# Kernel optimization log

Measured on AMD Instinct MI355X. Metric: run time of the kernel, lower is better.

Reference implementation:

```python
import jax, jax.numpy as jnp
import numpy as np

HSIZE = 128
E = 640000


def _init_linear(key, fan_in, fan_out):
    # torch nn.Linear default init: U(-1/sqrt(fan_in), 1/sqrt(fan_in))
    kw, kb = jax.random.split(key)
    bound = 1.0 / np.sqrt(fan_in)
    W = jax.random.uniform(kw, (fan_in, fan_out), jnp.float32, -bound, bound)
    b = jax.random.uniform(kb, (fan_out,), jnp.float32, -bound, bound)
    return W, b


def setup_inputs() -> dict:
    key = jax.random.key(0)
    ks = jax.random.split(key, 6)
    hself = jax.random.normal(ks[0], (E, HSIZE), jnp.float32)
    hother = jax.random.normal(ks[1], (E, HSIZE), jnp.float32)
    Wm1, bm1 = _init_linear(ks[2], 2 * HSIZE, HSIZE)
    Wm2, bm2 = _init_linear(ks[3], HSIZE, HSIZE)
    Wu1, bu1 = _init_linear(ks[4], 2 * HSIZE, HSIZE)
    Wu2, bu2 = _init_linear(ks[5], HSIZE, HSIZE)
    return {"hself": hself, "hother": hother,
            "Wm1": Wm1, "bm1": bm1, "Wm2": Wm2, "bm2": bm2,
            "Wu1": Wu1, "bu1": bu1, "Wu2": Wu2, "bu2": bu2}


def _mlp2(a, b, W1, b1, W2, b2):
    # concat([a, b], -1) @ W1 done without materializing the concat
    h = a @ W1[:HSIZE] + b @ W1[HSIZE:] + b1
    h = jax.nn.relu(h)
    return h @ W2 + b2


def reference(hself, hother, Wm1, bm1, Wm2, bm2, Wu1, bu1, Wu2, bu2):
    # msg: Linear(2h,h) -> ReLU -> Linear(h,h) on cat([hself, hother])
    msg = _mlp2(hself, hother, Wm1, bm1, Wm2, bm2)
    # upd: Linear(2h,h) -> ReLU -> Linear(h,h) on cat([hself, msg])
    out = _mlp2(hself, msg, Wu1, bu1, Wu2, bu2)
    return out
```

## Files before the change

kernel.cpp:

```cpp
#include <hip/hip_runtime.h>

typedef __bf16 bf16_t;
typedef __bf16 bf16x8 __attribute__((ext_vector_type(8)));
typedef float f32x4 __attribute__((ext_vector_type(4)));

#define MFMA(a, b, c) __builtin_amdgcn_mfma_f32_16x16x32_bf16((a), (b), (c), 0, 0, 0)

#define E_ROWS 640000
#define BM 128

static __device__ __forceinline__ bf16x8 cvt8(float4 a, float4 b) {
  bf16x8 r;
  r[0] = (bf16_t)a.x; r[1] = (bf16_t)a.y; r[2] = (bf16_t)a.z; r[3] = (bf16_t)a.w;
  r[4] = (bf16_t)b.x; r[5] = (bf16_t)b.y; r[6] = (bf16_t)b.z; r[7] = (bf16_t)b.w;
  return r;
}

__global__ __launch_bounds__(256) void prep_weights(
    const float* __restrict__ Wm1, const float* __restrict__ Wm2,
    const float* __restrict__ Wu1, const float* __restrict__ Wu2,
    bf16_t* __restrict__ wt) {
  int c = blockIdx.x * 256 + threadIdx.x;
  if (c >= 12288) return;
  int lane = c & 63, f = c >> 6;
  const float* W; int base;
  if (f < 64)       { W = Wm1; base = 0;   }
  else if (f < 96)  { W = Wm2; base = 64;  }
  else if (f < 160) { W = Wu1; base = 96;  }
  else              { W = Wu2; base = 160; }
  int fl = f - base;
  int ks = fl >> 3, nb = fl & 7;
  int k0 = 32 * ks + 8 * (lane >> 4);
  int n  = 16 * nb + (lane & 15);
  bf16x8 v;
  #pragma unroll
  for (int j = 0; j < 8; ++j) v[j] = (bf16_t)W[(size_t)(k0 + j) * 128 + n];
  ((bf16x8*)wt)[c] = v;
}

static __device__ __forceinline__ void loadB(bf16x8* dst, const bf16x8* gb,
                                             int fragbase, int lane) {
  #pragma unroll
  for (int n = 0; n < 8; ++n) dst[n] = gb[(size_t)(fragbase + n) * 64 + lane];
}

__global__ __launch_bounds__(256, 2) void fused_mp(
    const float* __restrict__ hself, const float* __restrict__ hother,
    const bf16_t* __restrict__ wt,
    const float* __restrict__ bm1, const float* __restrict__ bm2,
    const float* __restrict__ bu1, const float* __restrict__ bu2,
    float* __restrict__ out) {
  __shared__ bf16_t conv[128 * 128];

  const int tid = threadIdx.x;
  const int lane = tid & 63;
  const int wave = tid >> 6;
  const int col16 = lane & 15;
  const int kgrp = lane >> 4;
  const int rowloc0 = wave * 32;
  const int swz = (col16 & 7) << 4;

  const bf16x8* gb = (const bf16x8*)wt;

  float bm1v[8], bm2v[8], bu1v[8], bu2v[8];
  #pragma unroll
  for (int n = 0; n < 8; ++n) {
    bm1v[n] = bm1[n * 16 + col16];
    bm2v[n] = bm2[n * 16 + col16];
    bu1v[n] = bu1[n * 16 + col16];
    bu2v[n] = bu2[n * 16 + col16];
  }

  bf16x8 hsf[2][4], hof[2][4];
  {
    float4 t0[2][4], t1[2][4], u0[2][4], u1[2][4];
    #pragma unroll
    for (int rb = 0; rb < 2; ++rb) {
      #pragma unroll
      for (int ks = 0; ks < 4; ++ks) {
        size_t row = (size_t)blockIdx.x * BM + rowloc0 + rb * 16 + col16;
        const float* p = hself + row * 128 + ks * 32 + kgrp * 8;
        t0[rb][ks] = *(const float4*)p;
        t1[rb][ks] = *(const float4*)(p + 4);
        const float* q = hother + row * 128 + ks * 32 + kgrp * 8;
        u0[rb][ks] = *(const float4*)q;
        u1[rb][ks] = *(const float4*)(q + 4);
      }
    }
    #pragma unroll
    for (int rb = 0; rb < 2; ++rb) {
      #pragma unroll
      for (int ks = 0; ks < 4; ++ks) {
        hsf[rb][ks] = cvt8(t0[rb][ks], t1[rb][ks]);
        hof[rb][ks] = cvt8(u0[rb][ks], u1[rb][ks]);
      }
    }
  }

  f32x4 acc[2][8];
  bf16x8 bA[8], bB[8];

  #pragma unroll
  for (int rb = 0; rb < 2; ++rb)
    #pragma unroll
    for (int n = 0; n < 8; ++n)
      acc[rb][n] = (f32x4){0.f, 0.f, 0.f, 0.f};

  loadB(bA, gb, 0, lane);
  #pragma unroll
  for (int ks = 0; ks < 8; ++ks) {
    bf16x8* bc = (ks & 1) ? bB : bA;
    bf16x8* bn = (ks & 1) ? bA : bB;
    if (ks < 7) loadB(bn, gb, (ks + 1) * 8, lane);
    bf16x8 a0 = (ks < 4) ? hsf[0][ks & 3] : hof[0][ks & 3];
    bf16x8 a1 = (ks < 4) ? hsf[1][ks & 3] : hof[1][ks & 3];
    #pragma unroll
    for (int n = 0; n < 8; ++n) {
      acc[0][n] = MFMA(a0, bc[n], acc[0][n]);
      acc[1][n] = MFMA(a1, bc[n], acc[1][n]);
    }
  }

  #pragma unroll
  for (int rb = 0; rb < 2; ++rb)
    #pragma unroll
    for (int n = 0; n < 8; ++n)
      #pragma unroll
      for (int e = 0; e < 4; ++e) {
        float v = fmaxf(acc[rb][n][e] + bm1v[n], 0.f);
        int r = rowloc0 + rb * 16 + kgrp * 4 + e;
        int byteoff = ((r << 8) + (n * 16 + col16) * 2) ^ ((r & 7) << 4);
        *(bf16_t*)((char*)conv + byteoff) = (bf16_t)v;
      }
  asm volatile("s_waitcnt lgkmcnt(0)" ::: "memory");

  bf16x8 h1f[2][4];
  #pragma unroll
  for (int rb = 0; rb < 2; ++rb)
    #pragma unroll
    for (int ks = 0; ks < 4; ++ks) {
      int r = rowloc0 + rb * 16 + col16;
      h1f[rb][ks] = *(const bf16x8*)((const char*)conv +
                    (((r << 8) + ks * 64 + kgrp * 16) ^ swz));
    }

  #pragma unroll
  for (int rb = 0; rb < 2; ++rb)
    #pragma unroll
    for (int n = 0; n < 8; ++n)
      acc[rb][n] = (f32x4){0.f, 0.f, 0.f, 0.f};

  loadB(bA, gb, 64, lane);
  #pragma unroll
  for (int ks = 0; ks < 4; ++ks) {
    bf16x8* bc = (ks & 1) ? bB : bA;
    bf16x8* bn = (ks & 1) ? bA : bB;
    if (ks < 3) loadB(bn, gb, 64 + (ks + 1) * 8, lane);
    #pragma unroll
    for (int n = 0; n < 8; ++n) {
      acc[0][n] = MFMA(h1f[0][ks], bc[n], acc[0][n]);
      acc[1][n] = MFMA(h1f[1][ks], bc[n], acc[1][n]);
    }
  }

  #pragma unroll
  for (int rb = 0; rb < 2; ++rb)
    #pragma unroll
    for (int n = 0; n < 8; ++n)
      #pragma unroll
      for (int e = 0; e < 4; ++e) {
        float v = acc[rb][n][e] + bm2v[n];
        int r = rowloc0 + rb * 16 + kgrp * 4 + e;
        int byteoff = ((r << 8) + (n * 16 + col16) * 2) ^ ((r & 7) << 4);
        *(bf16_t*)((char*)conv + byteoff) = (bf16_t)v;
      }
  asm volatile("s_waitcnt lgkmcnt(0)" ::: "memory");

  bf16x8 msgf[2][4];
  #pragma unroll
  for (int rb = 0; rb < 2; ++rb)
    #pragma unroll
    for (int ks = 0; ks < 4; ++ks) {
      int r = rowloc0 + rb * 16 + col16;
      msgf[rb][ks] = *(const bf16x8*)((const char*)conv +
                     (((r << 8) + ks * 64 + kgrp * 16) ^ swz));
    }

  #pragma unroll
  for (int rb = 0; rb < 2; ++rb)
    #pragma unroll
    for (int n = 0; n < 8; ++n)
      acc[rb][n] = (f32x4){0.f, 0.f, 0.f, 0.f};

  loadB(bA, gb, 96, lane);
  #pragma unroll
  for (int ks = 0; ks < 8; ++ks) {
    bf16x8* bc = (ks & 1) ? bB : bA;
    bf16x8* bn = (ks & 1) ? bA : bB;
    if (ks < 7) loadB(bn, gb, 96 + (ks + 1) * 8, lane);
    bf16x8 a0 = (ks < 4) ? hsf[0][ks & 3] : msgf[0][ks & 3];
    bf16x8 a1 = (ks < 4) ? hsf[1][ks & 3] : msgf[1][ks & 3];
    #pragma unroll
    for (int n = 0; n < 8; ++n) {
      acc[0][n] = MFMA(a0, bc[n], acc[0][n]);
      acc[1][n] = MFMA(a1, bc[n], acc[1][n]);
    }
  }

  #pragma unroll
  for (int rb = 0; rb < 2; ++rb)
    #pragma unroll
    for (int n = 0; n < 8; ++n)
      #pragma unroll
      for (int e = 0; e < 4; ++e) {
        float v = fmaxf(acc[rb][n][e] + bu1v[n], 0.f);
        int r = rowloc0 + rb * 16 + kgrp * 4 + e;
        int byteoff = ((r << 8) + (n * 16 + col16) * 2) ^ ((r & 7) << 4);
        *(bf16_t*)((char*)conv + byteoff) = (bf16_t)v;
      }
  asm volatile("s_waitcnt lgkmcnt(0)" ::: "memory");

  bf16x8 h2f[2][4];
  #pragma unroll
  for (int rb = 0; rb < 2; ++rb)
    #pragma unroll
    for (int ks = 0; ks < 4; ++ks) {
      int r = rowloc0 + rb * 16 + col16;
      h2f[rb][ks] = *(const bf16x8*)((const char*)conv +
                    (((r << 8) + ks * 64 + kgrp * 16) ^ swz));
    }

  #pragma unroll
  for (int rb = 0; rb < 2; ++rb)
    #pragma unroll
    for (int n = 0; n < 8; ++n)
      acc[rb][n] = (f32x4){0.f, 0.f, 0.f, 0.f};

  loadB(bA, gb, 160, lane);
  #pragma unroll
  for (int ks = 0; ks < 4; ++ks) {
    bf16x8* bc = (ks & 1) ? bB : bA;
    bf16x8* bn = (ks & 1) ? bA : bB;
    if (ks < 3) loadB(bn, gb, 160 + (ks + 1) * 8, lane);
    #pragma unroll
    for (int n = 0; n < 8; ++n) {
      acc[0][n] = MFMA(h2f[0][ks], bc[n], acc[0][n]);
      acc[1][n] = MFMA(h2f[1][ks], bc[n], acc[1][n]);
    }
  }

  #pragma unroll
  for (int rb = 0; rb < 2; ++rb)
    #pragma unroll
    for (int n = 0; n < 8; ++n)
      #pragma unroll
      for (int e = 0; e < 4; ++e) {
        size_t r = (size_t)blockIdx.x * BM + rowloc0 + rb * 16 + kgrp * 4 + e;
        out[r * 128 + n * 16 + col16] = acc[rb][n][e] + bu2v[n];
      }
}

extern "C" void kernel_launch(void* const* d_in, const int* in_sizes, int n_in,
                              void* d_out, int out_size, void* d_ws, size_t ws_size,
                              hipStream_t stream) {
  const float* hself  = (const float*)d_in[0];
  const float* hother = (const float*)d_in[1];
  const float* Wm1 = (const float*)d_in[2];
  const float* bm1 = (const float*)d_in[3];
  const float* Wm2 = (const float*)d_in[4];
  const float* bm2 = (const float*)d_in[5];
  const float* Wu1 = (const float*)d_in[6];
  const float* bu1 = (const float*)d_in[7];
  const float* Wu2 = (const float*)d_in[8];
  const float* bu2 = (const float*)d_in[9];
  float* out = (float*)d_out;
  bf16_t* wt = (bf16_t*)d_ws;

  prep_weights<<<48, 256, 0, stream>>>(Wm1, Wm2, Wu1, Wu2, wt);
  fused_mp<<<E_ROWS / BM, 256, 0, stream>>>(hself, hother, wt,
                                            bm1, bm2, bu1, bu2, out);
}
```

Measured before the change: 350.1 us.

## Swap MFMA operands to compute transposed tiles, vectorize stores and repack

Swaps the MFMA operands so each wave computes the transposed output tile, with weights as the A operand and activations as the B operand. Each lane then holds four consecutive output columns of one row. The final fp32 output is written with float4 stores instead of scalar stores. Inter-layer activations are repacked through per-wave LDS with packed 8-byte writes instead of per-element bf16 stores. Bias is folded into the accumulator initialization. The new layout must match the MFMA fragment convention exactly for the results to stay correct.

```diff
diff --git a/kernel.cpp b/kernel.cpp
--- a/kernel.cpp
+++ b/kernel.cpp
@@ -14,6 +14,12 @@
   r[0] = (bf16_t)a.x; r[1] = (bf16_t)a.y; r[2] = (bf16_t)a.z; r[3] = (bf16_t)a.w;
   r[4] = (bf16_t)b.x; r[5] = (bf16_t)b.y; r[6] = (bf16_t)b.z; r[7] = (bf16_t)b.w;
   return r;
+}
+
+static __device__ __forceinline__ unsigned int pk2(float a, float b) {
+  unsigned short ua = __builtin_bit_cast(unsigned short, (bf16_t)a);
+  unsigned short ub = __builtin_bit_cast(unsigned short, (bf16_t)b);
+  return ((unsigned int)ub << 16) | ua;
 }
 
 __global__ __launch_bounds__(256) void prep_weights(
@@ -38,10 +44,10 @@
   ((bf16x8*)wt)[c] = v;
 }
 
-static __device__ __forceinline__ void loadB(bf16x8* dst, const bf16x8* gb,
+static __device__ __forceinline__ void loadW(bf16x8* dst, const bf16x8* gb,
                                              int fragbase, int lane) {
   #pragma unroll
-  for (int n = 0; n < 8; ++n) dst[n] = gb[(size_t)(fragbase + n) * 64 + lane];
+  for (int n = 0; n < 8; ++n) dst[n] = gb[(fragbase + n) * 64 + lane];
 }
 
 __global__ __launch_bounds__(256, 2) void fused_mp(
@@ -50,214 +56,196 @@
     const float* __restrict__ bm1, const float* __restrict__ bm2,
     const float* __restrict__ bu1, const float* __restrict__ bu2,
     float* __restrict__ out) {
-  __shared__ bf16_t conv[128 * 128];
+  __shared__ bf16_t repack[4 * 4096];
 
   const int tid = threadIdx.x;
   const int lane = tid & 63;
   const int wave = tid >> 6;
-  const int col16 = lane & 15;
-  const int kgrp = lane >> 4;
-  const int rowloc0 = wave * 32;
-  const int swz = (col16 & 7) << 4;
-
+  const int c = lane & 15;
+  const int g = lane >> 4;
+
+  char* myrep = (char*)(repack + wave * 4096);
   const bf16x8* gb = (const bf16x8*)wt;
-
-  float bm1v[8], bm2v[8], bu1v[8], bu2v[8];
-  #pragma unroll
-  for (int n = 0; n < 8; ++n) {
-    bm1v[n] = bm1[n * 16 + col16];
-    bm2v[n] = bm2[n * 16 + col16];
-    bu1v[n] = bu1[n * 16 + col16];
-    bu2v[n] = bu2[n * 16 + col16];
-  }
+  const size_t rowbase = (size_t)blockIdx.x * BM + wave * 32;
 
   bf16x8 hsf[2][4], hof[2][4];
   {
     float4 t0[2][4], t1[2][4], u0[2][4], u1[2][4];
     #pragma unroll
-    for (int rb = 0; rb < 2; ++rb) {
+    for (int mt = 0; mt < 2; ++mt) {
       #pragma unroll
       for (int ks = 0; ks < 4; ++ks) {
-        size_t row = (size_t)blockIdx.x * BM + rowloc0 + rb * 16 + col16;
-        const float* p = hself + row * 128 + ks * 32 + kgrp * 8;
-        t0[rb][ks] = *(const float4*)p;
-        t1[rb][ks] = *(const float4*)(p + 4);
-        const float* q = hother + row * 128 + ks * 32 + kgrp * 8;
-        u0[rb][ks] = *(const float4*)q;
-        u1[rb][ks] = *(const float4*)(q + 4);
+        size_t row = rowbase + mt * 16 + c;
+        const float* p = hself + row * 128 + ks * 32 + g * 8;
+        t0[mt][ks] = *(const float4*)p;
+        t1[mt][ks] = *(const float4*)(p + 4);
+        const float* q = hother + row * 128 + ks * 32 + g * 8;
+        u0[mt][ks] = *(const float4*)q;
+        u1[mt][ks] = *(const float4*)(q + 4);
       }
     }
     #pragma unroll
-    for (int rb = 0; rb < 2; ++rb) {
+    for (int mt = 0; mt < 2; ++mt) {
       #pragma unroll
       for (int ks = 0; ks < 4; ++ks) {
-        hsf[rb][ks] = cvt8(t0[rb][ks], t1[rb][ks]);
-        hof[rb][ks] = cvt8(u0[rb][ks], u1[rb][ks]);
+        hsf[mt][ks] = cvt8(t0[mt][ks], t1[mt][ks]);
+        hof[mt][ks] = cvt8(u0[mt][ks], u1[mt][ks]);
       }
     }
   }
 
   f32x4 acc[2][8];
-  bf16x8 bA[8], bB[8];
-
-  #pragma unroll
-  for (int rb = 0; rb < 2; ++rb)
-    #pragma unroll
-    for (int n = 0; n < 8; ++n)
-      acc[rb][n] = (f32x4){0.f, 0.f, 0.f, 0.f};
-
-  loadB(bA, gb, 0, lane);
+  bf16x8 wA[8], wB[8];
+
+  #pragma unroll
+  for (int nb = 0; nb < 8; ++nb) {
+    float4 b4 = *(const float4*)(bm1 + nb * 16 + g * 4);
+    acc[0][nb] = (f32x4){b4.x, b4.y, b4.z, b4.w};
+    acc[1][nb] = acc[0][nb];
+  }
+  loadW(wA, gb, 0, lane);
   #pragma unroll
   for (int ks = 0; ks < 8; ++ks) {
-    bf16x8* bc = (ks & 1) ? bB : bA;
-    bf16x8* bn = (ks & 1) ? bA : bB;
-    if (ks < 7) loadB(bn, gb, (ks + 1) * 8, lane);
-    bf16x8 a0 = (ks < 4) ? hsf[0][ks & 3] : hof[0][ks & 3];
-    bf16x8 a1 = (ks < 4) ? hsf[1][ks & 3] : hof[1][ks & 3];
-    #pragma unroll
-    for (int n = 0; n < 8; ++n) {
-      acc[0][n] = MFMA(a0, bc[n], acc[0][n]);
-      acc[1][n] = MFMA(a1, bc[n], acc[1][n]);
-    }
-  }
-
-  #pragma unroll
-  for (int rb = 0; rb < 2; ++rb)
-    #pragma unroll
-    for (int n = 0; n < 8; ++n)
-      #pragma unroll
-      for (int e = 0; e < 4; ++e) {
-        float v = fmaxf(acc[rb][n][e] + bm1v[n], 0.f);
-        int r = rowloc0 + rb * 16 + kgrp * 4 + e;
-        int byteoff = ((r << 8) + (n * 16 + col16) * 2) ^ ((r & 7) << 4);
-        *(bf16_t*)((char*)conv + byteoff) = (bf16_t)v;
-      }
+    bf16x8* wc = (ks & 1) ? wB : wA;
+    bf16x8* wn = (ks & 1) ? wA : wB;
+    if (ks < 7) loadW(wn, gb, (ks + 1) * 8, lane);
+    bf16x8 x0 = (ks < 4) ? hsf[0][ks & 3] : hof[0][ks & 3];
+    bf16x8 x1 = (ks < 4) ? hsf[1][ks & 3] : hof[1][ks & 3];
+    #pragma unroll
+    for (int nb = 0; nb < 8; ++nb) {
+      acc[0][nb] = MFMA(wc[nb], x0, acc[0][nb]);
+      acc[1][nb] = MFMA(wc[nb], x1, acc[1][nb]);
+    }
+  }
+
+  #pragma unroll
+  for (int mt = 0; mt < 2; ++mt)
+    #pragma unroll
+    for (int nb = 0; nb < 8; ++nb) {
+      f32x4 v = acc[mt][nb];
+      uint2 w;
+      w.x = pk2(fmaxf(v[0], 0.f), fmaxf(v[1], 0.f));
+      w.y = pk2(fmaxf(v[2], 0.f), fmaxf(v[3], 0.f));
+      int dstlane = c + 16 * (2 * (nb & 1) + (g >> 1));
+      int off = ((mt * 4 + (nb >> 1)) * 64 + dstlane) * 16 + (g & 1) * 8;
+      *(uint2*)(myrep + off) = w;
+    }
   asm volatile("s_waitcnt lgkmcnt(0)" ::: "memory");
-
-  bf16x8 h1f[2][4];
-  #pragma unroll
-  for (int rb = 0; rb < 2; ++rb)
-    #pragma unroll
-    for (int ks = 0; ks < 4; ++ks) {
-      int r = rowloc0 + rb * 16 + col16;
-      h1f[rb][ks] = *(const bf16x8*)((const char*)conv +
-                    (((r << 8) + ks * 64 + kgrp * 16) ^ swz));
-    }
-
-  #pragma unroll
-  for (int rb = 0; rb < 2; ++rb)
-    #pragma unroll
-    for (int n = 0; n < 8; ++n)
-      acc[rb][n] = (f32x4){0.f, 0.f, 0.f, 0.f};
-
-  loadB(bA, gb, 64, lane);
+  bf16x8 h1B[2][4];
+  #pragma unroll
+  for (int mt = 0; mt < 2; ++mt)
+    #pragma unroll
+    for (int ks = 0; ks < 4; ++ks)
+      h1B[mt][ks] = *(const bf16x8*)(myrep + ((mt * 4 + ks) * 64 + lane) * 16);
+
+  #pragma unroll
+  for (int nb = 0; nb < 8; ++nb) {
+    float4 b4 = *(const float4*)(bm2 + nb * 16 + g * 4);
+    acc[0][nb] = (f32x4){b4.x, b4.y, b4.z, b4.w};
+    acc[1][nb] = acc[0][nb];
+  }
+  loadW(wA, gb, 64, lane);
   #pragma unroll
   for (int ks = 0; ks < 4; ++ks) {
-    bf16x8* bc = (ks & 1) ? bB : bA;
-    bf16x8* bn = (ks & 1) ? bA : bB;
-    if (ks < 3) loadB(bn, gb, 64 + (ks + 1) * 8, lane);
-    #pragma unroll
-    for (int n = 0; n < 8; ++n) {
-      acc[0][n] = MFMA(h1f[0][ks], bc[n], acc[0][n]);
-      acc[1][n] = MFMA(h1f[1][ks], bc[n], acc[1][n]);
-    }
-  }
-
-  #pragma unroll
-  for (int rb = 0; rb < 2; ++rb)
-    #pragma unroll
-    for (int n = 0; n < 8; ++n)
-      #pragma unroll
-      for (int e = 0; e < 4; ++e) {
-        float v = acc[rb][n][e] + bm2v[n];
-        int r = rowloc0 + rb * 16 + kgrp * 4 + e;
-        int byteoff = ((r << 8) + (n * 16 + col16) * 2) ^ ((r & 7) << 4);
-        *(bf16_t*)((char*)conv + byteoff) = (bf16_t)v;
-      }
+    bf16x8* wc = (ks & 1) ? wB : wA;
+    bf16x8* wn = (ks & 1) ? wA : wB;
+    if (ks < 3) loadW(wn, gb, 64 + (ks + 1) * 8, lane);
+    #pragma unroll
+    for (int nb = 0; nb < 8; ++nb) {
+      acc[0][nb] = MFMA(wc[nb], h1B[0][ks], acc[0][nb]);
+      acc[1][nb] = MFMA(wc[nb], h1B[1][ks], acc[1][nb]);
+    }
+  }
+
+  #pragma unroll
+  for (int mt = 0; mt < 2; ++mt)
+    #pragma unroll
+    for (int nb = 0; nb < 8; ++nb) {
+      f32x4 v = acc[mt][nb];
+      uint2 w;
+      w.x = pk2(v[0], v[1]);
+      w.y = pk2(v[2], v[3]);
+      int dstlane = c + 16 * (2 * (nb & 1) + (g >> 1));
+      int off = ((mt * 4 + (nb >> 1)) * 64 + dstlane) * 16 + (g & 1) * 8;
+      *(uint2*)(myrep + off) = w;
+    }
   asm volatile("s_waitcnt lgkmcnt(0)" ::: "memory");
-
-  bf16x8 msgf[2][4];
-  #pragma unroll
-  for (int rb = 0; rb < 2; ++rb)
-    #pragma unroll
-    for (int ks = 0; ks < 4; ++ks) {
-      int r = rowloc0 + rb * 16 + col16;
-      msgf[rb][ks] = *(const bf16x8*)((const char*)conv +
-                     (((r << 8) + ks * 64 + kgrp * 16) ^ swz));
-    }
-
-  #pragma unroll
-  for (int rb = 0; rb < 2; ++rb)
-    #pragma unroll
-    for (int n = 0; n < 8; ++n)
-      acc[rb][n] = (f32x4){0.f, 0.f, 0.f, 0.f};
-
-  loadB(bA, gb, 96, lane);
+  bf16x8 msgB[2][4];
+  #pragma unroll
+  for (int mt = 0; mt < 2; ++mt)
+    #pragma unroll
+    for (int ks = 0; ks < 4; ++ks)
+      msgB[mt][ks] = *(const bf16x8*)(myrep + ((mt * 4 + ks) * 64 + lane) * 16);
+
+  #pragma unroll
+  for (int nb = 0; nb < 8; ++nb) {
+    float4 b4 = *(const float4*)(bu1 + nb * 16 + g * 4);
+    acc[0][nb] = (f32x4){b4.x, b4.y, b4.z, b4.w};
+    acc[1][nb] = acc[0][nb];
+  }
+  loadW(wA, gb, 96, lane);
   #pragma unroll
   for (int ks = 0; ks < 8; ++ks) {
-    bf16x8* bc = (ks & 1) ? bB : bA;
-    bf16x8* bn = (ks & 1) ? bA : bB;
-    if (ks < 7) loadB(bn, gb, 96 + (ks + 1) * 8, lane);
-    bf16x8 a0 = (ks < 4) ? hsf[0][ks & 3] : msgf[0][ks & 3];
-    bf16x8 a1 = (ks < 4) ? hsf[1][ks & 3] : msgf[1][ks & 3];
-    #pragma unroll
-    for (int n = 0; n < 8; ++n) {
-      acc[0][n] = MFMA(a0, bc[n], acc[0][n]);
-      acc[1][n] = MFMA(a1, bc[n], acc[1][n]);
-    }
-  }
-
-  #pragma unroll
-  for (int rb = 0; rb < 2; ++rb)
-    #pragma unroll
-    for (int n = 0; n < 8; ++n)
-      #pragma unroll
-      for (int e = 0; e < 4; ++e) {
-        float v = fmaxf(acc[rb][n][e] + bu1v[n], 0.f);
-        int r = rowloc0 + rb * 16 + kgrp * 4 + e;
-        int byteoff = ((r << 8) + (n * 16 + col16) * 2) ^ ((r & 7) << 4);
-        *(bf16_t*)((char*)conv + byteoff) = (bf16_t)v;
-      }
+    bf16x8* wc = (ks & 1) ? wB : wA;
+    bf16x8* wn = (ks & 1) ? wA : wB;
+    if (ks < 7) loadW(wn, gb, 96 + (ks + 1) * 8, lane);
+    bf16x8 x0 = (ks < 4) ? hsf[0][ks & 3] : msgB[0][ks & 3];
+    bf16x8 x1 = (ks < 4) ? hsf[1][ks & 3] : msgB[1][ks & 3];
+    #pragma unroll
+    for (int nb = 0; nb < 8; ++nb) {
+      acc[0][nb] = MFMA(wc[nb], x0, acc[0][nb]);
+      acc[1][nb] = MFMA(wc[nb], x1, acc[1][nb]);
+    }
+  }
+
+  #pragma unroll
+  for (int mt = 0; mt < 2; ++mt)
+    #pragma unroll
+    for (int nb = 0; nb < 8; ++nb) {
+      f32x4 v = acc[mt][nb];
+      uint2 w;
+      w.x = pk2(fmaxf(v[0], 0.f), fmaxf(v[1], 0.f));
+      w.y = pk2(fmaxf(v[2], 0.f), fmaxf(v[3], 0.f));
+      int dstlane = c + 16 * (2 * (nb & 1) + (g >> 1));
+      int off = ((mt * 4 + (nb >> 1)) * 64 + dstlane) * 16 + (g & 1) * 8;
+      *(uint2*)(myrep + off) = w;
+    }
   asm volatile("s_waitcnt lgkmcnt(0)" ::: "memory");
-
-  bf16x8 h2f[2][4];
-  #pragma unroll
-  for (int rb = 0; rb < 2; ++rb)
-    #pragma unroll
-    for (int ks = 0; ks < 4; ++ks) {
-      int r = rowloc0 + rb * 16 + col16;
-      h2f[rb][ks] = *(const bf16x8*)((const char*)conv +
-                    (((r << 8) + ks * 64 + kgrp * 16) ^ swz));
-    }
-
-  #pragma unroll
-  for (int rb = 0; rb < 2; ++rb)
-    #pragma unroll
-    for (int n = 0; n < 8; ++n)
-      acc[rb][n] = (f32x4){0.f, 0.f, 0.f, 0.f};
-
-  loadB(bA, gb, 160, lane);
+  bf16x8 h2B[2][4];
+  #pragma unroll
+  for (int mt = 0; mt < 2; ++mt)
+    #pragma unroll
+    for (int ks = 0; ks < 4; ++ks)
+      h2B[mt][ks] = *(const bf16x8*)(myrep + ((mt * 4 + ks) * 64 + lane) * 16);
+
+  #pragma unroll
+  for (int nb = 0; nb < 8; ++nb) {
+    float4 b4 = *(const float4*)(bu2 + nb * 16 + g * 4);
+    acc[0][nb] = (f32x4){b4.x, b4.y, b4.z, b4.w};
+    acc[1][nb] = acc[0][nb];
+  }
+  loadW(wA, gb, 160, lane);
   #pragma unroll
   for (int ks = 0; ks < 4; ++ks) {
-    bf16x8* bc = (ks & 1) ? bB : bA;
-    bf16x8* bn = (ks & 1) ? bA : bB;
-    if (ks < 3) loadB(bn, gb, 160 + (ks + 1) * 8, lane);
-    #pragma unroll
-    for (int n = 0; n < 8; ++n) {
-      acc[0][n] = MFMA(h2f[0][ks], bc[n], acc[0][n]);
-      acc[1][n] = MFMA(h2f[1][ks], bc[n], acc[1][n]);
-    }
-  }
-
-  #pragma unroll
-  for (int rb = 0; rb < 2; ++rb)
-    #pragma unroll
-    for (int n = 0; n < 8; ++n)
-      #pragma unroll
-      for (int e = 0; e < 4; ++e) {
-        size_t r = (size_t)blockIdx.x * BM + rowloc0 + rb * 16 + kgrp * 4 + e;
-        out[r * 128 + n * 16 + col16] = acc[rb][n][e] + bu2v[n];
-      }
+    bf16x8* wc = (ks & 1) ? wB : wA;
+    bf16x8* wn = (ks & 1) ? wA : wB;
+    if (ks < 3) loadW(wn, gb, 160 + (ks + 1) * 8, lane);
+    #pragma unroll
+    for (int nb = 0; nb < 8; ++nb) {
+      acc[0][nb] = MFMA(wc[nb], h2B[0][ks], acc[0][nb]);
+      acc[1][nb] = MFMA(wc[nb], h2B[1][ks], acc[1][nb]);
+    }
+  }
+
+  #pragma unroll
+  for (int mt = 0; mt < 2; ++mt)
+    #pragma unroll
+    for (int nb = 0; nb < 8; ++nb) {
+      size_t row = rowbase + mt * 16 + c;
+      f32x4 v = acc[mt][nb];
+      *(float4*)(out + row * 128 + nb * 16 + g * 4) =
+          (float4){v[0], v[1], v[2], v[3]};
+    }
 }
 
 extern "C" void kernel_launch(void* const* d_in, const int* in_sizes, int n_in,
```

Result: faster. 335.4 us (-4.2%).
